# Optimization experiments

Measured on AMD Instinct MI355X. Metric: run time of the kernel, lower is better.

Reference implementation:

```python
import jax, jax.numpy as jnp
import numpy as np

NUM_ARG = 2
NUM_IN = 4096
NUM_OUT = 4096
NUM_BLK = NUM_IN // NUM_ARG          # 2048 logic blocks
B_OUT = NUM_OUT // NUM_BLK           # 2 outputs per block
NUM_CORNER = 2 ** NUM_ARG            # 4 belief-table entries per gate
N_SLOW = 8192


def _hadamard_like(n):
    # H recursion from Logic.__init__: H -> [[H, -H], [H, H]]
    H = np.ones((1, 1), np.float32)
    for _ in range(n):
        H = np.block([[H, -H], [H, H]])
    return jnp.asarray(H)  # (2^n, 2^n)


def _corner_signs(n):
    # corner r, arg i: s = +1 if bit i of r set else -1 (consistent with H recursion)
    k = np.arange(2 ** n)
    bits = (k[:, None] >> np.arange(n)) & 1
    return jnp.asarray(2.0 * bits - 1.0, dtype=jnp.float32)  # (2^n, n)


def setup_inputs() -> dict:
    key = jax.random.key(0)
    kx, kp = jax.random.split(key)
    X = jax.random.normal(kx, (N_SLOW, NUM_IN), dtype=jnp.float32)
    P = jax.random.normal(kp, (NUM_CORNER, NUM_OUT), dtype=jnp.float32)
    return {"X": X, "P": P}


def reference(X, P):
    # Belief table: corner values of the multilinear polynomial parameterized by P
    H = _hadamard_like(NUM_ARG)                      # (2^nAr, 2^nAr)
    B = H @ P                                        # (2^nAr, nOut)
    Bb = B.reshape(NUM_CORNER, NUM_BLK, B_OUT)       # per-block belief tables

    Xb = X.reshape(-1, NUM_BLK, NUM_ARG)             # (nSlow, nBlk, nAr), nFast = 1
    S = _corner_signs(NUM_ARG)                       # (2^nAr, nAr)

    # Multilinear hypercube interpolation weights over [-1, 1]^nAr:
    # w[s, b, c] = prod_i (1 + s_i(c) * x_i) / 2
    w = jnp.prod((1.0 + Xb[:, :, None, :] * S[None, None, :, :]) * 0.5, axis=-1)
    # (nSlow, nBlk, 2^nAr)

    Y = jnp.einsum('sbc,cbo->sbo', w, Bb)            # (nSlow, nBlk, bOut)
    return Y.reshape(X.shape[0], NUM_OUT)
```

## Files before the change

kernel.cpp:

```cpp
#include <hip/hip_runtime.h>


#define NUM_IN 4096
#define N_SLOW 8192

__global__ __launch_bounds__(256) void logic_poly_kernel(
    const float* __restrict__ X,
    const float* __restrict__ P,
    float* __restrict__ Y,
    int rows_per_chunk)
{
    const int col4 = (blockIdx.x & 3) * 256 + threadIdx.x;
    const int c0   = col4 * 4;

    const float4 p0 = *reinterpret_cast<const float4*>(P + 0 * NUM_IN + c0);
    const float4 p1 = *reinterpret_cast<const float4*>(P + 1 * NUM_IN + c0);
    const float4 p2 = *reinterpret_cast<const float4*>(P + 2 * NUM_IN + c0);
    const float4 p3 = *reinterpret_cast<const float4*>(P + 3 * NUM_IN + c0);

    const int row_begin = (blockIdx.x >> 2) * rows_per_chunk;
    const int row_end   = min(row_begin + rows_per_chunk, N_SLOW);

    for (int s = row_begin; s < row_end; ++s) {
        const size_t off = (size_t)s * NUM_IN + c0;
        const float4 x = *reinterpret_cast<const float4*>(X + off);

        const float x01 = x.x * x.y;
        const float x23 = x.z * x.w;

        float4 y;
        y.x = p0.x + p1.x * x.x + p2.x * x.y + p3.x * x01;
        y.y = p0.y + p1.y * x.x + p2.y * x.y + p3.y * x01;
        y.z = p0.z + p1.z * x.z + p2.z * x.w + p3.z * x23;
        y.w = p0.w + p1.w * x.z + p2.w * x.w + p3.w * x23;

        *reinterpret_cast<float4*>(Y + off) = y;
    }
}

extern "C" void kernel_launch(void* const* d_in, const int* in_sizes, int n_in,
                              void* d_out, int out_size, void* d_ws, size_t ws_size,
                              hipStream_t stream) {
    const float* X = (const float*)d_in[0];
    const float* P = (const float*)d_in[1];
    float* Y = (float*)d_out;

    const int ROWS_PER_CHUNK = 32;
    const int n_chunks = (N_SLOW + ROWS_PER_CHUNK - 1) / ROWS_PER_CHUNK;
    dim3 grid(4 * n_chunks);
    dim3 block(256);
    logic_poly_kernel<<<grid, block, 0, stream>>>(X, P, Y, ROWS_PER_CHUNK);
}
```

Before: 52.46 us.

## Unroll row loop with compile-time chunk size and nontemporal output stores

Makes the rows-per-chunk a compile-time constant (halved to 16, doubling the grid) and fully unrolls the row loop, processing two rows per iteration so several X loads can be in flight at once. Output writes use nontemporal stores to avoid polluting cache with streamed Y data. The kernel is purely bandwidth-bound (128 MB+128 MB traffic), so gains depend on better memory-level parallelism and store behavior; the bounds check is removed, relying on N_SLOW being divisible by the chunk size.

Result: faster. 44.19 us (-15.8%).

```diff
diff --git a/kernel.cpp b/kernel.cpp
--- a/kernel.cpp
+++ b/kernel.cpp
@@ -3,38 +3,54 @@
 
 #define NUM_IN 4096
 #define N_SLOW 8192
+#define ROWS_PER_CHUNK 16
+
+typedef float f32x4 __attribute__((ext_vector_type(4)));
 
 __global__ __launch_bounds__(256) void logic_poly_kernel(
     const float* __restrict__ X,
     const float* __restrict__ P,
-    float* __restrict__ Y,
-    int rows_per_chunk)
+    float* __restrict__ Y)
 {
     const int col4 = (blockIdx.x & 3) * 256 + threadIdx.x;
     const int c0   = col4 * 4;
 
-    const float4 p0 = *reinterpret_cast<const float4*>(P + 0 * NUM_IN + c0);
-    const float4 p1 = *reinterpret_cast<const float4*>(P + 1 * NUM_IN + c0);
-    const float4 p2 = *reinterpret_cast<const float4*>(P + 2 * NUM_IN + c0);
-    const float4 p3 = *reinterpret_cast<const float4*>(P + 3 * NUM_IN + c0);
+    const f32x4 p0 = *reinterpret_cast<const f32x4*>(P + 0 * NUM_IN + c0);
+    const f32x4 p1 = *reinterpret_cast<const f32x4*>(P + 1 * NUM_IN + c0);
+    const f32x4 p2 = *reinterpret_cast<const f32x4*>(P + 2 * NUM_IN + c0);
+    const f32x4 p3 = *reinterpret_cast<const f32x4*>(P + 3 * NUM_IN + c0);
 
-    const int row_begin = (blockIdx.x >> 2) * rows_per_chunk;
-    const int row_end   = min(row_begin + rows_per_chunk, N_SLOW);
+    const int row_begin = (blockIdx.x >> 2) * ROWS_PER_CHUNK;
 
-    for (int s = row_begin; s < row_end; ++s) {
-        const size_t off = (size_t)s * NUM_IN + c0;
-        const float4 x = *reinterpret_cast<const float4*>(X + off);
+    #pragma unroll
+    for (int u = 0; u < ROWS_PER_CHUNK / 2; ++u) {
+        const int s0 = row_begin + 2 * u;
+        const size_t offA = (size_t)s0 * NUM_IN + c0;
+        const size_t offB = offA + NUM_IN;
 
-        const float x01 = x.x * x.y;
-        const float x23 = x.z * x.w;
+        const f32x4 xa = *reinterpret_cast<const f32x4*>(X + offA);
+        const f32x4 xb = *reinterpret_cast<const f32x4*>(X + offB);
 
-        float4 y;
-        y.x = p0.x + p1.x * x.x + p2.x * x.y + p3.x * x01;
-        y.y = p0.y + p1.y * x.x + p2.y * x.y + p3.y * x01;
-        y.z = p0.z + p1.z * x.z + p2.z * x.w + p3.z * x23;
-        y.w = p0.w + p1.w * x.z + p2.w * x.w + p3.w * x23;
+        f32x4 ya, yb;
+        {
+            const float m01 = xa.x * xa.y;
+            const float m23 = xa.z * xa.w;
+            ya.x = p0.x + p1.x * xa.x + p2.x * xa.y + p3.x * m01;
+            ya.y = p0.y + p1.y * xa.x + p2.y * xa.y + p3.y * m01;
+            ya.z = p0.z + p1.z * xa.z + p2.z * xa.w + p3.z * m23;
+            ya.w = p0.w + p1.w * xa.z + p2.w * xa.w + p3.w * m23;
+        }
+        {
+            const float m01 = xb.x * xb.y;
+            const float m23 = xb.z * xb.w;
+            yb.x = p0.x + p1.x * xb.x + p2.x * xb.y + p3.x * m01;
+            yb.y = p0.y + p1.y * xb.x + p2.y * xb.y + p3.y * m01;
+            yb.z = p0.z + p1.z * xb.z + p2.z * xb.w + p3.z * m23;
+            yb.w = p0.w + p1.w * xb.z + p2.w * xb.w + p3.w * m23;
+        }
 
-        *reinterpret_cast<float4*>(Y + off) = y;
+        __builtin_nontemporal_store(ya, reinterpret_cast<f32x4*>(Y + offA));
+        __builtin_nontemporal_store(yb, reinterpret_cast<f32x4*>(Y + offB));
     }
 }
 
@@ -45,9 +61,8 @@
     const float* P = (const float*)d_in[1];
     float* Y = (float*)d_out;
 
-    const int ROWS_PER_CHUNK = 32;
-    const int n_chunks = (N_SLOW + ROWS_PER_CHUNK - 1) / ROWS_PER_CHUNK;
+    const int n_chunks = N_SLOW / ROWS_PER_CHUNK;
     dim3 grid(4 * n_chunks);
     dim3 block(256);
-    logic_poly_kernel<<<grid, block, 0, stream>>>(X, P, Y, ROWS_PER_CHUNK);
+    logic_poly_kernel<<<grid, block, 0, stream>>>(X, P, Y);
 }
```
